# Kernel tuning notes

Hardware: AMD Instinct MI355X
Metric: run time of the kernel (lower is better)

Reference implementation:

```python
import jax, jax.numpy as jnp
import numpy as np

BINS = 100
NORMALIZE = False
SIGMA = 1.0
B, N = 128, 512
EDGE_P = 0.02  # edge probability -> avg degree ~10


def _make_adj(key):
    u = jax.random.uniform(key, (B, N, N))
    a = (u < EDGE_P).astype(jnp.float32)
    up = jnp.triu(a, 1)
    return up + jnp.swapaxes(up, -1, -2)  # symmetric, zero diagonal


def setup_inputs() -> dict:
    key = jax.random.key(0)
    k1, k2 = jax.random.split(key)
    return {"adj_1": _make_adj(k1), "adj_2": _make_adj(k2)}


def _clustering_hist(adj):
    # adj: [B, N, N] binary symmetric, zero diag
    deg = adj.sum(-1)                                   # [B, N]
    a2 = jnp.matmul(adj, adj)                           # [B, N, N]
    tri2 = jnp.einsum('bij,bji->bi', a2, adj)           # diag(A^3) = 2 * triangles
    denom = deg * (deg - 1.0)
    # nx.clustering: c_i = 2*T_i / (k_i*(k_i-1)) = diag(A^3)_i / (k_i*(k_i-1)); 0 if k_i < 2
    c = jnp.where(denom > 0, tri2 / jnp.maximum(denom, 1.0), 0.0)  # [B, N] in [0,1]
    # histogram over [0,1] with BINS bins; value 1.0 falls in last bin (torch.histogram semantics)
    idx = jnp.clip((c * BINS).astype(jnp.int32), 0, BINS - 1)
    hist = jax.vmap(lambda ix: jnp.zeros((BINS,), jnp.float32).at[ix].add(1.0))(idx)
    if NORMALIZE:
        hist = hist * (BINS / N)  # density: count / (n_samples * bin_width)
    return hist  # [B, BINS]


def _rbf_mmd(x, y, sigma):
    # biased MMD^2 estimate with RBF kernel
    def kmat(a, b):
        sq = (a * a).sum(-1)[:, None] + (b * b).sum(-1)[None, :] - 2.0 * (a @ b.T)
        return jnp.exp(-jnp.maximum(sq, 0.0) / (2.0 * sigma * sigma))
    return kmat(x, x).mean() + kmat(y, y).mean() - 2.0 * kmat(x, y).mean()


def reference(adj_1, adj_2):
    h1 = _clustering_hist(adj_1)
    h2 = _clustering_hist(adj_2)
    return _rbf_mmd(h1, h2, SIGMA)
```

## Files before the change

kernel.cpp:

```cpp
#include <hip/hip_runtime.h>
#include <stdint.h>

#define BATCH 128
#define NN 512
#define BINS 100
#define WORDS 8
#define WPAD 9
#define ECAP 6144

__global__ __launch_bounds__(1024) void k_cluster_hist(
    const float* __restrict__ adj1, const float* __restrict__ adj2,
    float* __restrict__ hist )
{
    __shared__ unsigned long long bits[NN][WPAD];
    __shared__ unsigned int edges[ECAP];
    __shared__ int tri2[NN];
    __shared__ int histI[BINS];
    __shared__ int ecnt;

    const int gb = blockIdx.x;
    const float* __restrict__ g =
        (gb < BATCH ? adj1 : adj2) + (size_t)(gb & (BATCH - 1)) * NN * NN;

    const int tid  = threadIdx.x;
    const int lane = tid & 63;
    const int wave = tid >> 6;

    if (tid < BINS) histI[tid] = 0;
    if (tid < NN)   tri2[tid]  = 0;
    if (tid == 0)   ecnt = 0;

    #pragma unroll 2
    for (int r = wave; r < NN; r += 16) {
        const float* rowp = g + (size_t)r * NN;
        #pragma unroll
        for (int seg = 0; seg < 2; ++seg) {
            float4 v = *(const float4*)(rowp + seg * 256 + 4 * lane);
            unsigned long long m0 = __ballot(v.x != 0.0f);
            unsigned long long m1 = __ballot(v.y != 0.0f);
            unsigned long long m2 = __ballot(v.z != 0.0f);
            unsigned long long m3 = __ballot(v.w != 0.0f);
            if (lane == 0) {
                bits[r][seg * 4 + 0] = m0;
                bits[r][seg * 4 + 1] = m1;
                bits[r][seg * 4 + 2] = m2;
                bits[r][seg * 4 + 3] = m3;
            }
        }
    }
    __syncthreads();

    for (int p = tid; p < NN * WORDS; p += 1024) {
        int r = p >> 3;
        int m = p & 7;
        unsigned long long w = bits[r][m];
        while (w) {
            int L = __builtin_ctzll(w);
            w &= w - 1;
            int j = ((m >> 2) << 8) + 4 * L + (m & 3);
            if (j > r) {
                int slot = atomicAdd(&ecnt, 1);
                if (slot < ECAP) edges[slot] = ((unsigned)r << 10) | (unsigned)j;
            }
        }
    }
    __syncthreads();

    const int ne = ecnt < ECAP ? ecnt : ECAP;
    for (int e = tid; e < ne; e += 1024) {
        unsigned ed = edges[e];
        int i = ed >> 10;
        int j = ed & 1023;
        int acc = 0;
        #pragma unroll
        for (int w = 0; w < WORDS; ++w)
            acc += __popcll(bits[i][w] & bits[j][w]);
        atomicAdd(&tri2[i], acc);
        atomicAdd(&tri2[j], acc);
    }
    __syncthreads();

    if (tid < NN) {
        int deg = 0;
        #pragma unroll
        for (int w = 0; w < WORDS; ++w) deg += __popcll(bits[tid][w]);
        float t2    = (float)tri2[tid];
        float degf  = (float)deg;
        float denom = degf * (degf - 1.0f);
        float c = denom > 0.0f ? t2 / denom : 0.0f;
        int idx = (int)(c * 100.0f);
        idx = idx < 0 ? 0 : (idx > BINS - 1 ? BINS - 1 : idx);
        atomicAdd(&histI[idx], 1);
    }
    __syncthreads();

    if (tid < BINS) hist[(size_t)gb * BINS + tid] = (float)histI[tid];
}

__global__ __launch_bounds__(256) void k_mmd_partial(
    const float* __restrict__ hist, float* __restrict__ partials)
{
    int p = blockIdx.x * 256 + threadIdx.x;
    int t   = p >> 14;
    int rem = p & 16383;
    int i = rem >> 7;
    int j = rem & 127;
    const float4* x4;
    const float4* y4;
    float w;
    if (t == 0)      { x4 = (const float4*)(hist + (size_t)i * BINS);           y4 = (const float4*)(hist + (size_t)j * BINS);           w =  1.0f; }
    else if (t == 1) { x4 = (const float4*)(hist + (size_t)(BATCH + i) * BINS); y4 = (const float4*)(hist + (size_t)(BATCH + j) * BINS); w =  1.0f; }
    else             { x4 = (const float4*)(hist + (size_t)i * BINS);           y4 = (const float4*)(hist + (size_t)(BATCH + j) * BINS); w = -2.0f; }
    float sq = 0.0f;
    #pragma unroll
    for (int k = 0; k < BINS / 4; ++k) {
        float4 a = x4[k];
        float4 b = y4[k];
        float d0 = a.x - b.x, d1 = a.y - b.y, d2 = a.z - b.z, d3 = a.w - b.w;
        sq += d0 * d0 + d1 * d1 + d2 * d2 + d3 * d3;
    }
    float local = w * expf(-0.5f * sq);

    __shared__ float red[256];
    red[threadIdx.x] = local;
    __syncthreads();
    for (int s = 128; s >= 1; s >>= 1) {
        if (threadIdx.x < s) red[threadIdx.x] += red[threadIdx.x + s];
        __syncthreads();
    }
    if (threadIdx.x == 0) partials[blockIdx.x] = red[0];
}

__global__ __launch_bounds__(64) void k_mmd_final(
    const float* __restrict__ partials, float* __restrict__ out, int nparts)
{
    int lane = threadIdx.x;
    float v = 0.0f;
    for (int p = lane; p < nparts; p += 64) v += partials[p];
    #pragma unroll
    for (int off = 32; off >= 1; off >>= 1) v += __shfl_xor(v, off, 64);
    if (lane == 0) out[0] = v * (1.0f / (float)(BATCH * BATCH));
}

extern "C" void kernel_launch(void* const* d_in, const int* in_sizes, int n_in,
                              void* d_out, int out_size, void* d_ws, size_t ws_size,
                              hipStream_t stream) {
    const float* a1 = (const float*)d_in[0];
    const float* a2 = (const float*)d_in[1];
    float* hist     = (float*)d_ws;
    float* partials = (float*)((char*)d_ws + 2 * BATCH * BINS * sizeof(float));
    float* out      = (float*)d_out;

    hipLaunchKernelGGL(k_cluster_hist, dim3(2 * BATCH), dim3(1024), 0, stream,
                       a1, a2, hist);
    hipLaunchKernelGGL(k_mmd_partial, dim3(192), dim3(256), 0, stream,
                       hist, partials);
    hipLaunchKernelGGL(k_mmd_final, dim3(1), dim3(64), 0, stream,
                       partials, out, 192);
}
```

Baseline: 282.8 us.

## Batch row loads per wave and replace per-edge atomics with wave prefix-sum compaction

```diff
diff --git a/kernel.cpp b/kernel.cpp
--- a/kernel.cpp
+++ b/kernel.cpp
@@ -30,21 +30,29 @@
     if (tid < NN)   tri2[tid]  = 0;
     if (tid == 0)   ecnt = 0;
 
-    #pragma unroll 2
-    for (int r = wave; r < NN; r += 16) {
-        const float* rowp = g + (size_t)r * NN;
+    for (int r0 = wave * 32; r0 < wave * 32 + 32; r0 += 8) {
+        float4 v[16];
         #pragma unroll
-        for (int seg = 0; seg < 2; ++seg) {
-            float4 v = *(const float4*)(rowp + seg * 256 + 4 * lane);
-            unsigned long long m0 = __ballot(v.x != 0.0f);
-            unsigned long long m1 = __ballot(v.y != 0.0f);
-            unsigned long long m2 = __ballot(v.z != 0.0f);
-            unsigned long long m3 = __ballot(v.w != 0.0f);
-            if (lane == 0) {
-                bits[r][seg * 4 + 0] = m0;
-                bits[r][seg * 4 + 1] = m1;
-                bits[r][seg * 4 + 2] = m2;
-                bits[r][seg * 4 + 3] = m3;
+        for (int i = 0; i < 8; ++i) {
+            const float* rowp = g + (size_t)(r0 + i) * NN + 4 * lane;
+            v[2 * i + 0] = *(const float4*)(rowp);
+            v[2 * i + 1] = *(const float4*)(rowp + 256);
+        }
+        #pragma unroll
+        for (int i = 0; i < 8; ++i) {
+            #pragma unroll
+            for (int s = 0; s < 2; ++s) {
+                float4 q = v[2 * i + s];
+                unsigned long long m0 = __ballot(q.x != 0.0f);
+                unsigned long long m1 = __ballot(q.y != 0.0f);
+                unsigned long long m2 = __ballot(q.z != 0.0f);
+                unsigned long long m3 = __ballot(q.w != 0.0f);
+                if (lane == 0) {
+                    bits[r0 + i][s * 4 + 0] = m0;
+                    bits[r0 + i][s * 4 + 1] = m1;
+                    bits[r0 + i][s * 4 + 2] = m2;
+                    bits[r0 + i][s * 4 + 3] = m3;
+                }
             }
         }
     }
@@ -54,14 +62,33 @@
         int r = p >> 3;
         int m = p & 7;
         unsigned long long w = bits[r][m];
-        while (w) {
-            int L = __builtin_ctzll(w);
-            w &= w - 1;
-            int j = ((m >> 2) << 8) + 4 * L + (m & 3);
-            if (j > r) {
-                int slot = atomicAdd(&ecnt, 1);
-                if (slot < ECAP) edges[slot] = ((unsigned)r << 10) | (unsigned)j;
-            }
+        int jbase = ((m >> 2) << 8) + (m & 3);
+        unsigned long long wm = w;
+        int d = r - jbase;
+        if (d >= 0) {
+            int Lmin = (d >> 2) + 1;
+            wm = (Lmin >= 64) ? 0ull : (w & (~0ull << Lmin));
+        }
+        int cnt = __popcll(wm);
+
+        int x = cnt;
+        #pragma unroll
+        for (int off = 1; off < 64; off <<= 1) {
+            int y = __shfl_up(x, off, 64);
+            if (lane >= off) x += y;
+        }
+        int excl = x - cnt;
+        int base = 0;
+        if (lane == 63) base = atomicAdd(&ecnt, x);
+        base = __shfl(base, 63, 64);
+
+        int idx = base + excl;
+        while (wm) {
+            int L = __builtin_ctzll(wm);
+            wm &= wm - 1;
+            int j = jbase + 4 * L;
+            if (idx < ECAP) edges[idx] = ((unsigned)r << 10) | (unsigned)j;
+            ++idx;
         }
     }
     __syncthreads();
```

New measurement: 290.0 us. 1.03x slower.
